# Kernel optimization log

Measured on AMD Instinct MI355X. Metric: run time of the kernel, lower is better.

## Reference

```python
import jax, jax.numpy as jnp
import numpy as np

DIM = 256
NUM_HEADS = 4
HEAD_DIM = DIM // NUM_HEADS  # 64
SCALE = HEAD_DIM ** -0.5


def _dwconv(x, w, b):
    # x: [B,H,W,C], w: [3,3,1,C] depthwise, stride 2, padding 1
    c = x.shape[-1]
    y = jax.lax.conv_general_dilated(
        x, w, window_strides=(2, 2), padding=((1, 1), (1, 1)),
        dimension_numbers=('NHWC', 'HWIO', 'NHWC'), feature_group_count=c)
    return y + b


def setup_inputs() -> dict:
    key = jax.random.key(0)
    ks = jax.random.split(key, 12)
    s = 0.02
    return {
        'x': jax.random.normal(ks[0], (8, 64, 64, DIM), jnp.float32),
        'q_w': jax.random.normal(ks[1], (DIM, DIM), jnp.float32) * s,
        'q_b': jnp.zeros((DIM,), jnp.float32),
        'k_w': jax.random.normal(ks[2], (DIM, HEAD_DIM), jnp.float32) * s,
        'k_b': jnp.zeros((HEAD_DIM,), jnp.float32),
        'v_w': jax.random.normal(ks[3], (DIM, HEAD_DIM), jnp.float32) * s,
        'v_b': jnp.zeros((HEAD_DIM,), jnp.float32),
        'kconv_w': jax.random.normal(ks[4], (3, 3, 1, HEAD_DIM), jnp.float32) * s,
        'kconv_b': jnp.zeros((HEAD_DIM,), jnp.float32),
        'vconv_w': jax.random.normal(ks[5], (3, 3, 1, HEAD_DIM), jnp.float32) * s,
        'vconv_b': jnp.zeros((HEAD_DIM,), jnp.float32),
        'out_w': jax.random.normal(ks[6], (DIM, DIM), jnp.float32) * s,
        'out_b': jnp.zeros((DIM,), jnp.float32),
    }


def reference(x, q_w, q_b, k_w, k_b, v_w, v_b,
              kconv_w, kconv_b, vconv_w, vconv_b, out_w, out_b):
    B, H, W, _ = x.shape
    S = H * W
    q = x @ q_w + q_b                      # [B,H,W,DIM]
    k = x @ k_w + k_b                      # [B,H,W,HEAD_DIM]
    v = x @ v_w + v_b
    k = _dwconv(k, kconv_w, kconv_b)       # [B,H/2,W/2,HEAD_DIM]
    v = _dwconv(v, vconv_w, vconv_b)
    Kv = (H // 2) * (W // 2)
    q = q.reshape(B, S, NUM_HEADS, HEAD_DIM)
    k = k.reshape(B, Kv, HEAD_DIM)
    v = v.reshape(B, Kv, HEAD_DIM)
    # MQA: single shared K/V head
    attn = jnp.einsum('bqhd,bkd->bhqk', q, k) * SCALE
    attn = jax.nn.softmax(attn, axis=-1)
    out = jnp.einsum('bhqk,bkd->bqhd', attn, v)   # [B,S,nh,hd]
    out = out.reshape(B, S, DIM) @ out_w + out_b
    return out.reshape(B, H, W, DIM)
```

## Files before the change

kernel.cpp:

```cpp
#include <hip/hip_runtime.h>
#include <hip/hip_bf16.h>

typedef __bf16 v8bf __attribute__((ext_vector_type(8)));
typedef float f32x4 __attribute__((ext_vector_type(4)));
typedef float f32x16 __attribute__((ext_vector_type(16)));
typedef int v2i __attribute__((ext_vector_type(2)));
typedef int v4i __attribute__((ext_vector_type(4)));

#define MFMA16(a, b, c) __builtin_amdgcn_mfma_f32_16x16x32_bf16(a, b, c, 0, 0, 0)
#define MFMA32(a, b, c) __builtin_amdgcn_mfma_f32_32x32x16_bf16(a, b, c, 0, 0, 0)
#define GLOAD16(gp, lp)                                                        \
  __builtin_amdgcn_global_load_lds(                                            \
      (const __attribute__((address_space(1))) void*)(gp),                     \
      (__attribute__((address_space(3))) void*)(lp), 16, 0, 0)

#define QSCALE 0.18033688011112042f

__global__ __launch_bounds__(256) void k_cvt_w(const float* __restrict__ qw,
                                               const float* __restrict__ kw,
                                               const float* __restrict__ vw,
                                               const float* __restrict__ ow,
                                               __bf16* __restrict__ wfrag,
                                               __bf16* __restrict__ owfrag) {
  int t = blockIdx.x * 256 + threadIdx.x;
  if (t < 98304) {
    int e = t & 7, idx = t >> 3;
    int l = idx & 63; idx >>= 6;
    int n = idx & 3; idx >>= 2;
    int kk = idx & 7, nb = idx >> 3;
    int nn = nb * 64 + n * 16 + (l & 15);
    int k = kk * 32 + 8 * (l >> 4) + e;
    float v;
    if (nn < 256) v = qw[k * 256 + nn] * QSCALE;
    else if (nn < 320) v = kw[k * 64 + (nn - 256)];
    else v = vw[k * 64 + (nn - 320)];
    wfrag[t] = (__bf16)v;
  } else {
    int u = t - 98304;
    int e = u & 7, idx = u >> 3;
    int l = idx & 63; idx >>= 6;
    int n = idx & 3; idx >>= 2;
    int kk = idx & 7, nb = idx >> 3;
    int nn = nb * 64 + n * 16 + (l & 15);
    int k = kk * 32 + 8 * (l >> 4) + e;
    owfrag[u] = (__bf16)ow[k * 256 + nn];
  }
}

__global__ __launch_bounds__(256) void k_qkv(const float* __restrict__ x,
                                             const __bf16* __restrict__ wfrag,
                                             const float* __restrict__ qb,
                                             const float* __restrict__ kb,
                                             const float* __restrict__ vb,
                                             __bf16* __restrict__ qo,
                                             __bf16* __restrict__ klin,
                                             __bf16* __restrict__ vlin) {
  int bx = blockIdx.x;
  int mb = (bx & 7) * 64 + (bx >> 3);
  int wave = threadIdx.x >> 6, lane = threadIdx.x & 63;
  int g = lane >> 4, c = lane & 15;
  int r0 = mb * 64 + wave * 16;
  const v8bf* wf = (const v8bf*)wfrag;

  v8bf a[8];
#pragma unroll
  for (int kk = 0; kk < 8; ++kk) {
    const float* ap = x + (size_t)(r0 + c) * 256 + kk * 32 + 8 * g;
    float4 f0 = *(const float4*)ap;
    float4 f1 = *(const float4*)(ap + 4);
    v8bf t;
    t[0] = (__bf16)f0.x; t[1] = (__bf16)f0.y; t[2] = (__bf16)f0.z; t[3] = (__bf16)f0.w;
    t[4] = (__bf16)f1.x; t[5] = (__bf16)f1.y; t[6] = (__bf16)f1.z; t[7] = (__bf16)f1.w;
    a[kk] = t;
  }
#pragma unroll
  for (int nb = 0; nb < 6; ++nb) {
    int n0 = nb * 64;
    f32x4 acc[4];
#pragma unroll
    for (int n = 0; n < 4; ++n) acc[n] = f32x4{0.f, 0.f, 0.f, 0.f};
#pragma unroll
    for (int kk = 0; kk < 8; ++kk) {
      v8bf bf[4];
#pragma unroll
      for (int n = 0; n < 4; ++n)
        bf[n] = wf[(((nb * 8 + kk) * 4 + n) << 6) | lane];
#pragma unroll
      for (int n = 0; n < 4; ++n) acc[n] = MFMA16(a[kk], bf[n], acc[n]);
    }
#pragma unroll
    for (int n = 0; n < 4; ++n) {
      int col = n0 + n * 16 + c;
      float bias;
      if (col < 256) bias = qb[col] * QSCALE;
      else if (col < 320) bias = kb[col - 256];
      else bias = vb[col - 320];
#pragma unroll
      for (int j = 0; j < 4; ++j) {
        int row = r0 + 4 * g + j;
        float v = acc[n][j] + bias;
        if (col < 256) qo[(size_t)row * 256 + col] = (__bf16)v;
        else if (col < 320) klin[(size_t)row * 64 + (col - 256)] = (__bf16)v;
        else vlin[(size_t)row * 64 + (col - 320)] = (__bf16)v;
      }
    }
  }
}

__global__ __launch_bounds__(256) void k_conv(const __bf16* __restrict__ klin,
                                              const __bf16* __restrict__ vlin,
                                              const float* __restrict__ kw,
                                              const float* __restrict__ kbias,
                                              const float* __restrict__ vw,
                                              const float* __restrict__ vbias,
                                              __bf16* __restrict__ kc,
                                              __bf16* __restrict__ vcT) {
  __shared__ __bf16 VT[32][66];
  int bx = blockIdx.x;
  int b = bx >> 5, pt = bx & 31;
  int t = threadIdx.x;
  int ch = t & 63, pg = t >> 6;
  float kwv[9], vwv[9];
#pragma unroll
  for (int i = 0; i < 9; ++i) { kwv[i] = kw[i * 64 + ch]; vwv[i] = vw[i * 64 + ch]; }
  float kb0 = kbias[ch], vb0 = vbias[ch];
  const __bf16* kin = klin + (size_t)b * 262144;
  const __bf16* vin = vlin + (size_t)b * 262144;
#pragma unroll
  for (int i = 0; i < 8; ++i) {
    int pl = pg * 8 + i;
    int p = pt * 32 + pl;
    int oy = p >> 5, ox = p & 31;
    float ak = kb0, av = vb0;
#pragma unroll
    for (int dy = 0; dy < 3; ++dy) {
      int iy = 2 * oy - 1 + dy;
      if (iy < 0 || iy > 63) continue;
#pragma unroll
      for (int dx = 0; dx < 3; ++dx) {
        int ix = 2 * ox - 1 + dx;
        if (ix < 0 || ix > 63) continue;
        size_t src = ((size_t)iy * 64 + ix) * 64 + ch;
        ak += (float)kin[src] * kwv[dy * 3 + dx];
        av += (float)vin[src] * vwv[dy * 3 + dx];
      }
    }
    kc[((size_t)b * 1024 + p) * 64 + ch] = (__bf16)ak;
    VT[pl][ch] = (__bf16)av;
  }
  __syncthreads();
  int row = t >> 2, c0 = (t & 3) * 8;
  __bf16 tmp[8];
#pragma unroll
  for (int i = 0; i < 8; ++i) tmp[i] = VT[c0 + i][row];
  *(v4i*)(vcT + (size_t)b * 65536 + row * 1024 + pt * 32 + c0) = *(v4i*)tmp;
}

__global__ __launch_bounds__(256) void k_attn(const __bf16* __restrict__ q,
                                              const __bf16* __restrict__ kc,
                                              const __bf16* __restrict__ vcT,
                                              const __bf16* __restrict__ owfrag,
                                              const float* __restrict__ ob,
                                              float* __restrict__ out) {
  __shared__ __bf16 SMEM[12288];
  int bx = blockIdx.x;
  int L = (bx & 7) * 128 + (bx >> 3);
  int b = L >> 7, qt = L & 127;
  int wave = threadIdx.x >> 6, lane = threadIdx.x & 63;
  int c = lane & 31, hi = lane >> 5;
  int t = threadIdx.x;
  size_t rowBase = (size_t)b * 4096 + qt * 32;

  int kj = t >> 5, kr = (t & 31) ^ kj;
  const __bf16* kg = kc + (size_t)b * 65536 + kr * 64 + kj * 8;
  int dt_ = t >> 7, ks_ = (t >> 6) & 1, vh_ = (t >> 5) & 1;
  int cc = (t & 31) ^ (ks_ * 2 + vh_);
  const __bf16* vg = vcT + (size_t)b * 65536 + (size_t)(dt_ * 32 + cc) * 1024 +
                     ks_ * 16 + vh_ * 8;
  __bf16* kl = &SMEM[t * 8];
  __bf16* vl = &SMEM[2048 + t * 8];

  int Koff[4], Voff[2][2];
#pragma unroll
  for (int kk = 0; kk < 4; ++kk) {
    int j = kk * 2 + hi;
    Koff[kk] = (j * 32 + (c ^ j)) * 8;
  }
#pragma unroll
  for (int ks = 0; ks < 2; ++ks)
#pragma unroll
    for (int dt = 0; dt < 2; ++dt) {
      int j = ks * 2 + hi;
      Voff[ks][dt] = (256 + dt * 128 + ks * 64 + hi * 32 + (c ^ j)) * 8;
    }

  const __bf16* qbase = q + (rowBase + c) * 256 + wave * 64 + hi * 8;
  v8bf Qf[4];
#pragma unroll
  for (int kk = 0; kk < 4; ++kk) Qf[kk] = *(const v8bf*)(qbase + kk * 16);

  f32x16 O0 = {}, O1 = {};
  const f32x16 Z16 = {};
  float ls0 = 0.f, ls1 = 0.f, ls2 = 0.f, ls3 = 0.f;

  GLOAD16(kg, kl);
  GLOAD16(vg, vl);
  GLOAD16(kg + 2048, kl + 4096);
  GLOAD16(vg + 32, vl + 4096);

  int cur = 0;
  int nxt2 = 2;
  for (int it = 0; it < 32; ++it) {
    if (it < 30) {
      GLOAD16(kg + (it + 2) * 2048, kl + nxt2 * 4096);
      GLOAD16(vg + (it + 2) * 32, vl + nxt2 * 4096);
      asm volatile("s_waitcnt vmcnt(4)" ::: "memory");
    } else if (it == 30) {
      asm volatile("s_waitcnt vmcnt(2)" ::: "memory");
    } else {
      asm volatile("s_waitcnt vmcnt(0)" ::: "memory");
    }
    __builtin_amdgcn_sched_barrier(0);
    __builtin_amdgcn_s_barrier();
    __builtin_amdgcn_sched_barrier(0);

    const __bf16* base = &SMEM[cur * 4096];
    v8bf Kf[4], Vf[2][2];
#pragma unroll
    for (int kk = 0; kk < 4; ++kk) Kf[kk] = *(const v8bf*)(base + Koff[kk]);
#pragma unroll
    for (int ks = 0; ks < 2; ++ks)
#pragma unroll
      for (int dt = 0; dt < 2; ++dt)
        Vf[ks][dt] = *(const v8bf*)(base + Voff[ks][dt]);

    f32x16 S = MFMA32(Kf[0], Qf[0], Z16);
    S = MFMA32(Kf[1], Qf[1], S);
    S = MFMA32(Kf[2], Qf[2], S);
    S = MFMA32(Kf[3], Qf[3], S);

#pragma unroll
    for (int r = 0; r < 16; ++r) S[r] = __builtin_amdgcn_exp2f(S[r]);
    ls0 += (S[0] + S[1]) + (S[2] + S[3]);
    ls1 += (S[4] + S[5]) + (S[6] + S[7]);
    ls2 += (S[8] + S[9]) + (S[10] + S[11]);
    ls3 += (S[12] + S[13]) + (S[14] + S[15]);

    int w[8];
#pragma unroll
    for (int q2 = 0; q2 < 8; ++q2) {
      int r;
      asm("v_cvt_pk_bf16_f32 %0, %1, %2"
          : "=v"(r) : "v"(S[2 * q2]), "v"(S[2 * q2 + 1]));
      w[q2] = r;
    }
    v2i s1 = __builtin_amdgcn_permlane32_swap(w[2], w[0], false, false);
    v2i s2 = __builtin_amdgcn_permlane32_swap(w[3], w[1], false, false);
    v2i s3 = __builtin_amdgcn_permlane32_swap(w[6], w[4], false, false);
    v2i s4 = __builtin_amdgcn_permlane32_swap(w[7], w[5], false, false);
    v4i pa0i, pa1i;
    pa0i[0] = s1[1]; pa0i[1] = s2[1]; pa0i[2] = s1[0]; pa0i[3] = s2[0];
    pa1i[0] = s3[1]; pa1i[1] = s4[1]; pa1i[2] = s3[0]; pa1i[3] = s4[0];
    v8bf pa0 = *(v8bf*)&pa0i, pa1 = *(v8bf*)&pa1i;

    O0 = MFMA32(pa0, Vf[0][0], O0);
    O1 = MFMA32(pa0, Vf[0][1], O1);
    O0 = MFMA32(pa1, Vf[1][0], O0);
    O1 = MFMA32(pa1, Vf[1][1], O1);

    cur = (cur == 2) ? 0 : cur + 1;
    nxt2 = (nxt2 == 2) ? 0 : nxt2 + 1;
  }

  float lsum = (ls0 + ls1) + (ls2 + ls3);
  float tot = lsum + __shfl_xor(lsum, 32);
  float linv = 1.0f / tot;

  __syncthreads();

  __bf16(*Ot)[264] = (__bf16(*)[264])SMEM;
#pragma unroll
  for (int r = 0; r < 16; ++r) {
    int qr = (r & 3) + 8 * (r >> 2) + 4 * hi;
    float li = __shfl(linv, qr);
    Ot[qr][wave * 64 + c] = (__bf16)(O0[r] * li);
    Ot[qr][wave * 64 + 32 + c] = (__bf16)(O1[r] * li);
  }
  __syncthreads();

  int g = lane >> 4, c16 = lane & 15;
  const v8bf* wf = (const v8bf*)owfrag;
  f32x4 acc[2][4];
#pragma unroll
  for (int m = 0; m < 2; ++m)
#pragma unroll
    for (int n = 0; n < 4; ++n) acc[m][n] = f32x4{0.f, 0.f, 0.f, 0.f};
#pragma unroll
  for (int kk = 0; kk < 8; ++kk) {
    v8bf a0 = *(const v8bf*)&Ot[c16][kk * 32 + 8 * g];
    v8bf a1 = *(const v8bf*)&Ot[16 + c16][kk * 32 + 8 * g];
    v8bf bf[4];
#pragma unroll
    for (int n = 0; n < 4; ++n)
      bf[n] = wf[(((wave * 8 + kk) * 4 + n) << 6) | lane];
#pragma unroll
    for (int n = 0; n < 4; ++n) {
      acc[0][n] = MFMA16(a0, bf[n], acc[0][n]);
      acc[1][n] = MFMA16(a1, bf[n], acc[1][n]);
    }
  }
#pragma unroll
  for (int n = 0; n < 4; ++n) {
    int col = wave * 64 + n * 16 + c16;
    float bias = ob[col];
#pragma unroll
    for (int m = 0; m < 2; ++m)
#pragma unroll
      for (int j = 0; j < 4; ++j) {
        int row = m * 16 + 4 * g + j;
        out[(rowBase + row) * 256 + col] = acc[m][n][j] + bias;
      }
  }
}

extern "C" void kernel_launch(void* const* d_in, const int* in_sizes, int n_in,
                              void* d_out, int out_size, void* d_ws, size_t ws_size,
                              hipStream_t stream) {
  const float* x   = (const float*)d_in[0];
  const float* qw  = (const float*)d_in[1];
  const float* qb  = (const float*)d_in[2];
  const float* kw  = (const float*)d_in[3];
  const float* kb  = (const float*)d_in[4];
  const float* vw  = (const float*)d_in[5];
  const float* vb  = (const float*)d_in[6];
  const float* kcw = (const float*)d_in[7];
  const float* kcb = (const float*)d_in[8];
  const float* vcw = (const float*)d_in[9];
  const float* vcb = (const float*)d_in[10];
  const float* ow  = (const float*)d_in[11];
  const float* ob  = (const float*)d_in[12];
  float* out = (float*)d_out;
  char* ws = (char*)d_ws;

  __bf16* qbuf   = (__bf16*)(ws + 16777216);
  __bf16* klin   = (__bf16*)(ws + 33554432);
  __bf16* vlin   = (__bf16*)(ws + 37748736);
  __bf16* kc     = (__bf16*)(ws + 41943040);
  __bf16* vcT    = (__bf16*)(ws + 42991616);
  __bf16* wfrag  = (__bf16*)(ws + 44040192);
  __bf16* owfrag = (__bf16*)(ws + 44236800);

  k_cvt_w<<<640, 256, 0, stream>>>(qw, kw, vw, ow, wfrag, owfrag);
  k_qkv<<<512, 256, 0, stream>>>(x, wfrag, qb, kb, vb, qbuf, klin, vlin);
  k_conv<<<256, 256, 0, stream>>>(klin, vlin, kcw, kcb, vcw, vcb, kc, vcT);
  k_attn<<<1024, 256, 0, stream>>>(qbuf, kc, vcT, owfrag, ob, out);
}
```

Baseline: 96.68 us.

## Pre-swizzle K/V tiles into contiguous blocks and move prefetch after barrier

```diff
diff --git a/kernel.cpp b/kernel.cpp
--- a/kernel.cpp
+++ b/kernel.cpp
@@ -156,9 +156,26 @@
   *(v4i*)(vcT + (size_t)b * 65536 + row * 1024 + pt * 32 + c0) = *(v4i*)tmp;
 }
 
+__global__ __launch_bounds__(256) void k_repack(const __bf16* __restrict__ kc,
+                                                const __bf16* __restrict__ vcT,
+                                                __bf16* __restrict__ kcS,
+                                                __bf16* __restrict__ vcS) {
+  int b = blockIdx.x >> 5, tile = blockIdx.x & 31;
+  int u = threadIdx.x;
+  int kj = u >> 5, kr = (u & 31) ^ kj;
+  v4i kv = *(const v4i*)(kc + (size_t)b * 65536 + (size_t)tile * 2048 +
+                         kr * 64 + kj * 8);
+  *(v4i*)(kcS + ((size_t)b * 32 + tile) * 2048 + u * 8) = kv;
+  int dt = u >> 7, ks = (u >> 6) & 1, vh = (u >> 5) & 1;
+  int cc = (u & 31) ^ (ks * 2 + vh);
+  v4i vv = *(const v4i*)(vcT + (size_t)b * 65536 + (size_t)(dt * 32 + cc) * 1024 +
+                         tile * 32 + ks * 16 + vh * 8);
+  *(v4i*)(vcS + ((size_t)b * 32 + tile) * 2048 + u * 8) = vv;
+}
+
 __global__ __launch_bounds__(256) void k_attn(const __bf16* __restrict__ q,
-                                              const __bf16* __restrict__ kc,
-                                              const __bf16* __restrict__ vcT,
+                                              const __bf16* __restrict__ kcS,
+                                              const __bf16* __restrict__ vcS,
                                               const __bf16* __restrict__ owfrag,
                                               const float* __restrict__ ob,
                                               float* __restrict__ out) {
@@ -171,12 +188,8 @@
   int t = threadIdx.x;
   size_t rowBase = (size_t)b * 4096 + qt * 32;
 
-  int kj = t >> 5, kr = (t & 31) ^ kj;
-  const __bf16* kg = kc + (size_t)b * 65536 + kr * 64 + kj * 8;
-  int dt_ = t >> 7, ks_ = (t >> 6) & 1, vh_ = (t >> 5) & 1;
-  int cc = (t & 31) ^ (ks_ * 2 + vh_);
-  const __bf16* vg = vcT + (size_t)b * 65536 + (size_t)(dt_ * 32 + cc) * 1024 +
-                     ks_ * 16 + vh_ * 8;
+  const __bf16* kg = kcS + (size_t)b * 65536 + t * 8;
+  const __bf16* vg = vcS + (size_t)b * 65536 + t * 8;
   __bf16* kl = &SMEM[t * 8];
   __bf16* vl = &SMEM[2048 + t * 8];
 
@@ -206,16 +219,12 @@
   GLOAD16(kg, kl);
   GLOAD16(vg, vl);
   GLOAD16(kg + 2048, kl + 4096);
-  GLOAD16(vg + 32, vl + 4096);
+  GLOAD16(vg + 2048, vl + 4096);
 
   int cur = 0;
   int nxt2 = 2;
   for (int it = 0; it < 32; ++it) {
-    if (it < 30) {
-      GLOAD16(kg + (it + 2) * 2048, kl + nxt2 * 4096);
-      GLOAD16(vg + (it + 2) * 32, vl + nxt2 * 4096);
-      asm volatile("s_waitcnt vmcnt(4)" ::: "memory");
-    } else if (it == 30) {
+    if (it < 31) {
       asm volatile("s_waitcnt vmcnt(2)" ::: "memory");
     } else {
       asm volatile("s_waitcnt vmcnt(0)" ::: "memory");
@@ -223,6 +232,10 @@
     __builtin_amdgcn_sched_barrier(0);
     __builtin_amdgcn_s_barrier();
     __builtin_amdgcn_sched_barrier(0);
+    if (it < 30) {
+      GLOAD16(kg + (it + 2) * 2048, kl + nxt2 * 4096);
+      GLOAD16(vg + (it + 2) * 2048, vl + nxt2 * 4096);
+    }
 
     const __bf16* base = &SMEM[cur * 4096];
     v8bf Kf[4], Vf[2][2];
@@ -342,6 +355,8 @@
   float* out = (float*)d_out;
   char* ws = (char*)d_ws;
 
+  __bf16* kcS    = (__bf16*)(ws + 0);
+  __bf16* vcS    = (__bf16*)(ws + 1048576);
   __bf16* qbuf   = (__bf16*)(ws + 16777216);
   __bf16* klin   = (__bf16*)(ws + 33554432);
   __bf16* vlin   = (__bf16*)(ws + 37748736);
@@ -353,5 +368,6 @@
   k_cvt_w<<<640, 256, 0, stream>>>(qw, kw, vw, ow, wfrag, owfrag);
   k_qkv<<<512, 256, 0, stream>>>(x, wfrag, qb, kb, vb, qbuf, klin, vlin);
   k_conv<<<256, 256, 0, stream>>>(klin, vlin, kcw, kcb, vcw, vcb, kc, vcT);
-  k_attn<<<1024, 256, 0, stream>>>(qbuf, kc, vcT, owfrag, ob, out);
-}
+  k_repack<<<256, 256, 0, stream>>>(kc, vcT, kcS, vcS);
+  k_attn<<<1024, 256, 0, stream>>>(qbuf, kcS, vcS, owfrag, ob, out);
+}
```

After: 95.56 us. No clear change (-1.2%).
